# Optimization experiments

Hardware: AMD Instinct MI355X
Metric: run time of the kernel (lower is better)

The kernel has to match this reference:

```python
import jax, jax.numpy as jnp
import numpy as np

B, S, D, H = 4, 1024, 1024, 16
HD = D // H  # head_dim = 64
MASKED_BIAS = -10000.0


def setup_inputs() -> dict:
    key = jax.random.key(0)
    ks = jax.random.split(key, 7)
    sc = 0.02
    return {
        "hidden_states": jax.random.normal(ks[0], (B, S, D), jnp.float32),
        "textual_key": jax.random.normal(ks[1], (B, H, S, HD), jnp.float32),
        "textual_value": jax.random.normal(ks[2], (B, H, S, HD), jnp.float32),
        "Wc": jax.random.normal(ks[3], (D, 3 * D), jnp.float32) * sc,  # Conv1D c_attn
        "bc": jnp.zeros((3 * D,), jnp.float32),
        "Wp": jax.random.normal(ks[4], (D, D), jnp.float32) * sc,  # Conv1D c_proj
        "bp": jnp.zeros((D,), jnp.float32),
    }


def reference(hidden_states, textual_key, textual_value, Wc, bc, Wp, bp):
    b, s, d = hidden_states.shape
    # Conv1D: x @ W + b, then split into q, k, v
    qkv = hidden_states @ Wc + bc  # [B,S,3D]
    q, k, v = jnp.split(qkv, 3, axis=-1)

    def split_heads(t):  # [B,S,D] -> [B,H,S,HD]
        return t.reshape(b, s, H, HD).transpose(0, 2, 1, 3)

    q, k, v = split_heads(q), split_heads(k), split_heads(v)

    # cross-key scores against textual past + fused elementwise self-term
    text_w = jnp.einsum("bhqd,bhkd->bhqk", q, textual_key)  # [B,H,S,S_kv]
    self_w = jnp.sum(q * k, axis=-1, keepdims=True)  # [B,H,S,1]
    attn_w = jnp.concatenate([text_w, self_w], axis=-1) / (HD ** 0.5)

    # nonResidual causal mask: bias[kl-ql:kl, 1:kl+1] (strict lower-tri since
    # columns are shifted by 1) concatenated with an always-true self column
    i = jnp.arange(s)
    causal = i[None, :] < i[:, None]  # [S,S_kv]: allow k < q (strict)
    mask = jnp.concatenate([causal, jnp.ones((s, 1), bool)], axis=-1)[None, None]
    attn_w = jnp.where(mask, attn_w, jnp.asarray(MASKED_BIAS, attn_w.dtype))
    attn_w = jax.nn.softmax(attn_w, axis=-1)

    w_rest, w_self = attn_w[..., :-1], attn_w[..., -1:]
    out = jnp.einsum("bhqk,bhkd->bhqd", w_rest, textual_value) + w_self * v

    out = out.transpose(0, 2, 1, 3).reshape(b, s, d)  # merge heads
    return out @ Wp + bp
```

## Files before the change

kernel.cpp:

```cpp
#include <hip/hip_runtime.h>

typedef __bf16 bf16_t;
typedef __bf16 bf16x8 __attribute__((ext_vector_type(8)));
typedef __bf16 bf16x4 __attribute__((ext_vector_type(4)));
typedef float f32x4 __attribute__((ext_vector_type(4)));

__device__ __forceinline__ void gl_lds16(const bf16_t* g, bf16_t* l) {
  __builtin_amdgcn_global_load_lds(
      (const __attribute__((address_space(1))) unsigned int*)g,
      (__attribute__((address_space(3))) unsigned int*)l, 16, 0, 0);
}

__global__ __launch_bounds__(256) void prep_kernel(
    const float* __restrict__ hs, const float* __restrict__ tk, const float* __restrict__ tv,
    const float* __restrict__ Wc, const float* __restrict__ Wp,
    bf16_t* __restrict__ Ahs, bf16_t* __restrict__ Ktb, bf16_t* __restrict__ Vtb,
    bf16_t* __restrict__ WcT, bf16_t* __restrict__ WpT) {
  const int blk = blockIdx.x;
  if (blk < 8192) {
    const float4* src = (blk < 4096) ? (const float4*)hs : (const float4*)tk;
    bf16x4* dst = (blk < 4096) ? (bf16x4*)Ahs : (bf16x4*)Ktb;
    int i = (blk & 4095) * 256 + threadIdx.x;
    float4 v = src[i];
    bf16x4 o;
    o[0] = (bf16_t)v.x; o[1] = (bf16_t)v.y; o[2] = (bf16_t)v.z; o[3] = (bf16_t)v.w;
    dst[i] = o;
  } else {
    __shared__ float tile[32][33];
    const int x = threadIdx.x & 31, y0 = threadIdx.x >> 5;
    const float* in; bf16_t* out; int R, C, c0, r0; size_t base;
    if (blk < 11264) {
      int t = blk - 8192; in = Wc; out = WcT; R = 1024; C = 3072; base = 0;
      c0 = (t % 96) * 32; r0 = (t / 96) * 32;
    } else if (blk < 12288) {
      int t = blk - 11264; in = Wp; out = WpT; R = 1024; C = 1024; base = 0;
      c0 = (t & 31) * 32; r0 = (t >> 5) * 32;
    } else {
      int t = blk - 12288; int z = t >> 6, rest = t & 63;
      in = tv; out = Vtb; R = 1024; C = 64; base = (size_t)z * 65536;
      c0 = (rest & 1) * 32; r0 = (rest >> 1) * 32;
    }
#pragma unroll
    for (int k = 0; k < 4; k++) {
      int y = y0 + 8 * k;
      tile[y][x] = in[base + (size_t)(r0 + y) * C + c0 + x];
    }
    __syncthreads();
#pragma unroll
    for (int k = 0; k < 4; k++) {
      int y = y0 + 8 * k;
      out[base + (size_t)(c0 + y) * R + r0 + x] = (bf16_t)tile[x][y];
    }
  }
}

__global__ __launch_bounds__(256) void gemm_qkv_kernel(
    const bf16_t* __restrict__ A, const bf16_t* __restrict__ Bt, const float* __restrict__ bias,
    bf16_t* __restrict__ Qo, bf16_t* __restrict__ Ko, bf16_t* __restrict__ Vo) {
  __shared__ __align__(16) bf16_t Asm[128 * 64];
  __shared__ __align__(16) bf16_t Bsm[128 * 64];
  const int tid = threadIdx.x;
  const int wave = tid >> 6, lane = tid & 63;
  const int c = lane & 15, qd = lane >> 4;
  const int wm = (wave & 1) * 64, wn = (wave >> 1) * 64;
  const int id = blockIdx.y * 24 + blockIdx.x;
  const int xcd = id & 7, idx = id >> 3;
  const int n0 = (xcd * 3 + (idx % 3)) * 128, m0 = (idx / 3) * 128;

  f32x4 acc[4][4];
#pragma unroll
  for (int i = 0; i < 4; i++)
#pragma unroll
    for (int j = 0; j < 4; j++) acc[i][j] = (f32x4){0.f, 0.f, 0.f, 0.f};

  for (int kt = 0; kt < 1024; kt += 64) {
#pragma unroll
    for (int p = 0; p < 4; p++) {
      int chunk = p * 256 + tid;
      int row = chunk >> 3, sb = chunk & 7;
      int kb = sb ^ (row & 7);
      gl_lds16(A + (size_t)(m0 + row) * 1024 + kt + kb * 8, &Asm[chunk * 8]);
      gl_lds16(Bt + (size_t)(n0 + row) * 1024 + kt + kb * 8, &Bsm[chunk * 8]);
    }
    __syncthreads();
#pragma unroll
    for (int kk = 0; kk < 2; kk++) {
      bf16x8 af[4], bfr[4];
#pragma unroll
      for (int i = 0; i < 4; i++) {
        int row = wm + 16 * i + c;
        af[i] = *(const bf16x8*)(&Asm[row * 64 + (((4 * kk + qd) ^ (row & 7)) << 3)]);
      }
#pragma unroll
      for (int j = 0; j < 4; j++) {
        int row = wn + 16 * j + c;
        bfr[j] = *(const bf16x8*)(&Bsm[row * 64 + (((4 * kk + qd) ^ (row & 7)) << 3)]);
      }
#pragma unroll
      for (int i = 0; i < 4; i++)
#pragma unroll
        for (int j = 0; j < 4; j++)
          acc[i][j] = __builtin_amdgcn_mfma_f32_16x16x32_bf16(af[i], bfr[j], acc[i][j], 0, 0, 0);
    }
    __syncthreads();
  }
#pragma unroll
  for (int j = 0; j < 4; j++) {
    int n = n0 + wn + 16 * j + c;
    float bv = bias[n];
    int type = n >> 10, d = n & 1023;
    int h = d >> 6, hd = d & 63;
    bf16_t* dst = (type == 0) ? Qo : (type == 1) ? Ko : Vo;
#pragma unroll
    for (int i = 0; i < 4; i++) {
#pragma unroll
      for (int r = 0; r < 4; r++) {
        int m = m0 + wm + 16 * i + 4 * qd + r;
        int bb = m >> 10, s = m & 1023;
        dst[(((size_t)bb * 16 + h) * 1024 + s) * 64 + hd] = (bf16_t)(acc[i][j][r] + bv);
      }
    }
  }
}

__global__ __launch_bounds__(256) void gemm_out_kernel(
    const bf16_t* __restrict__ A, const bf16_t* __restrict__ Bt, const float* __restrict__ bias,
    float* __restrict__ out) {
  __shared__ bf16_t Asm[2][8192];
  __shared__ bf16_t Bsm[2][8192];
  const int tid = threadIdx.x;
  const int wave = tid >> 6, lane = tid & 63;
  const int c = lane & 15, qd = lane >> 4;
  const int wm = (wave & 1) * 64, wn = (wave >> 1) * 64;
  const int m0 = blockIdx.y * 128, n0 = blockIdx.x * 128;

  f32x4 acc[4][4];
#pragma unroll
  for (int i = 0; i < 4; i++)
#pragma unroll
    for (int j = 0; j < 4; j++) acc[i][j] = (f32x4){0.f, 0.f, 0.f, 0.f};

#pragma unroll
  for (int p = 0; p < 4; p++) {
    int chunk = p * 256 + tid;
    int row = chunk >> 3, sb = chunk & 7;
    int kb = sb ^ (row & 7);
    gl_lds16(A + (size_t)(m0 + row) * 1024 + kb * 8, &Asm[0][chunk * 8]);
    gl_lds16(Bt + (size_t)(n0 + row) * 1024 + kb * 8, &Bsm[0][chunk * 8]);
  }
  for (int it = 0; it < 16; it++) {
    __syncthreads();
    if (it < 15) {
      int nbuf = (it + 1) & 1, kt = (it + 1) * 64;
#pragma unroll
      for (int p = 0; p < 4; p++) {
        int chunk = p * 256 + tid;
        int row = chunk >> 3, sb = chunk & 7;
        int kb = sb ^ (row & 7);
        gl_lds16(A + (size_t)(m0 + row) * 1024 + kt + kb * 8, &Asm[nbuf][chunk * 8]);
        gl_lds16(Bt + (size_t)(n0 + row) * 1024 + kt + kb * 8, &Bsm[nbuf][chunk * 8]);
      }
    }
    const int bs = it & 1;
#pragma unroll
    for (int kk = 0; kk < 2; kk++) {
      bf16x8 af[4], bfr[4];
#pragma unroll
      for (int i = 0; i < 4; i++) {
        int row = wm + 16 * i + c;
        af[i] = *(const bf16x8*)(&Asm[bs][row * 64 + (((4 * kk + qd) ^ (row & 7)) << 3)]);
      }
#pragma unroll
      for (int j = 0; j < 4; j++) {
        int row = wn + 16 * j + c;
        bfr[j] = *(const bf16x8*)(&Bsm[bs][row * 64 + (((4 * kk + qd) ^ (row & 7)) << 3)]);
      }
#pragma unroll
      for (int i = 0; i < 4; i++)
#pragma unroll
        for (int j = 0; j < 4; j++)
          acc[i][j] = __builtin_amdgcn_mfma_f32_16x16x32_bf16(af[i], bfr[j], acc[i][j], 0, 0, 0);
    }
  }
#pragma unroll
  for (int j = 0; j < 4; j++) {
    int n = n0 + wn + 16 * j + c;
    float bv = bias[n];
#pragma unroll
    for (int i = 0; i < 4; i++) {
#pragma unroll
      for (int r = 0; r < 4; r++) {
        int m = m0 + wm + 16 * i + 4 * qd + r;
        out[(size_t)m * 1024 + n] = acc[i][j][r] + bv;
      }
    }
  }
}

#define ATTN_M 12.0f
__global__ __launch_bounds__(512) void attn_kernel(
    const bf16_t* __restrict__ Q, const bf16_t* __restrict__ K, const bf16_t* __restrict__ V,
    const bf16_t* __restrict__ Ktxt, const bf16_t* __restrict__ VtxtT,
    bf16_t* __restrict__ Aout) {
  const int bh = blockIdx.x;
  const int qt = blockIdx.y;
  const int b = bh >> 4, h = bh & 15;
  const int tid = threadIdx.x, wave = tid >> 6, lane = tid & 63;
  const int c = lane & 15, qd = lane >> 4;
  const int i_base = qt * 128 + wave * 16;
  const int kt_max = 2 * qt + 1;

  const bf16_t* Qb = Q + (size_t)bh * 65536;
  const bf16_t* Kb = K + (size_t)bh * 65536;
  const bf16_t* Vb = V + (size_t)bh * 65536;
  const bf16_t* Ktb = Ktxt + (size_t)bh * 65536;
  const bf16_t* Vtb = VtxtT + (size_t)bh * 65536;

  __shared__ bf16_t Ksm[2][4096];
  __shared__ bf16_t Vsm[2][4096];
  __shared__ bf16_t Psm[8][1024];

  {
    int row = tid >> 3, sb = tid & 7, kb = sb ^ (row & 7);
    gl_lds16(Ktb + (size_t)row * 64 + kb * 8, &Ksm[0][tid * 8]);
    gl_lds16(Vtb + (size_t)row * 1024 + kb * 8, &Vsm[0][tid * 8]);
  }

  bf16x8 aq[2], kf0, kf1;
  {
    const size_t ro = (size_t)(i_base + c) * 64;
    aq[0] = *(const bf16x8*)(Qb + ro + 8 * qd);
    aq[1] = *(const bf16x8*)(Qb + ro + 32 + 8 * qd);
    kf0 = *(const bf16x8*)(Kb + ro + 8 * qd);
    kf1 = *(const bf16x8*)(Kb + ro + 32 + 8 * qd);
  }
  float part = 0.f;
#pragma unroll
  for (int jj = 0; jj < 8; jj++)
    part += (float)aq[0][jj] * (float)kf0[jj] + (float)aq[1][jj] * (float)kf1[jj];
  part += __shfl_xor(part, 16, 64);
  part += __shfl_xor(part, 32, 64);

  float wself[4], l_part[4];
  f32x4 O[4];
#pragma unroll
  for (int r = 0; r < 4; r++) {
    wself[r] = __expf(__shfl(part, 4 * qd + r, 64) * 0.125f - ATTN_M);
    l_part[r] = 0.f;
  }
#pragma unroll
  for (int t = 0; t < 4; t++)
#pragma unroll
    for (int r = 0; r < 4; r++)
      O[t][r] = wself[r] * (float)Vb[(size_t)(i_base + 4 * qd + r) * 64 + 16 * t + c];

  for (int kt = 0; kt <= kt_max; kt++) {
    __syncthreads();
    if (kt < kt_max) {
      int nb = (kt + 1) & 1;
      int row = tid >> 3, sb = tid & 7, kb = sb ^ (row & 7);
      gl_lds16(Ktb + (size_t)((kt + 1) * 64 + row) * 64 + kb * 8, &Ksm[nb][tid * 8]);
      gl_lds16(Vtb + (size_t)row * 1024 + (kt + 1) * 64 + kb * 8, &Vsm[nb][tid * 8]);
    }
    if (64 * kt >= i_base + 16) continue;
    const int bs = kt & 1;

    f32x4 sc[4];
#pragma unroll
    for (int t = 0; t < 4; t++) sc[t] = (f32x4){0.f, 0.f, 0.f, 0.f};
#pragma unroll
    for (int kk = 0; kk < 2; kk++) {
#pragma unroll
      for (int t = 0; t < 4; t++) {
        int row = 16 * t + c;
        bf16x8 bk = *(const bf16x8*)(&Ksm[bs][row * 64 + (((4 * kk + qd) ^ (row & 7)) << 3)]);
        sc[t] = __builtin_amdgcn_mfma_f32_16x16x32_bf16(aq[kk], bk, sc[t], 0, 0, 0);
      }
    }
    const bool edge = (64 * kt + 63 >= i_base);
    if (!edge) {
#pragma unroll
      for (int t = 0; t < 4; t++)
#pragma unroll
        for (int r = 0; r < 4; r++) {
          float p = __expf(sc[t][r] * 0.125f - ATTN_M);
          l_part[r] += p;
          sc[t][r] = p;
        }
    } else {
#pragma unroll
      for (int t = 0; t < 4; t++)
#pragma unroll
        for (int r = 0; r < 4; r++) {
          bool masked = (64 * kt + 16 * t + c >= i_base + 4 * qd + r);
          float p = masked ? 0.f : __expf(sc[t][r] * 0.125f - ATTN_M);
          l_part[r] += p;
          sc[t][r] = p;
        }
    }
#pragma unroll
    for (int t = 0; t < 4; t++) {
#pragma unroll
      for (int r = 0; r < 4; r++) {
        int row = 4 * qd + r;
        int col = 16 * t + c;
        Psm[wave][row * 64 + (((col >> 3) ^ (row & 7)) << 3) + (col & 7)] = (bf16_t)sc[t][r];
      }
    }
#pragma unroll
    for (int kk = 0; kk < 2; kk++) {
      bf16x8 ap = *(const bf16x8*)(&Psm[wave][c * 64 + (((4 * kk + qd) ^ (c & 7)) << 3)]);
#pragma unroll
      for (int u = 0; u < 4; u++) {
        int row = 16 * u + c;
        bf16x8 bv = *(const bf16x8*)(&Vsm[bs][row * 64 + (((4 * kk + qd) ^ (row & 7)) << 3)]);
        O[u] = __builtin_amdgcn_mfma_f32_16x16x32_bf16(ap, bv, O[u], 0, 0, 0);
      }
    }
  }

#pragma unroll
  for (int r = 0; r < 4; r++) {
#pragma unroll
    for (int mk = 1; mk < 16; mk <<= 1) l_part[r] += __shfl_xor(l_part[r], mk, 64);
    float inv = 1.0f / (l_part[r] + wself[r]);
    int i = i_base + 4 * qd + r;
#pragma unroll
    for (int u = 0; u < 4; u++)
      Aout[((size_t)b * 1024 + i) * 1024 + h * 64 + 16 * u + c] = (bf16_t)(O[u][r] * inv);
  }
}

extern "C" void kernel_launch(void* const* d_in, const int* in_sizes, int n_in,
                              void* d_out, int out_size, void* d_ws, size_t ws_size,
                              hipStream_t stream) {
  const float* hs = (const float*)d_in[0];
  const float* tk = (const float*)d_in[1];
  const float* tv = (const float*)d_in[2];
  const float* Wc = (const float*)d_in[3];
  const float* bc = (const float*)d_in[4];
  const float* Wp = (const float*)d_in[5];
  const float* bp = (const float*)d_in[6];
  float* out = (float*)d_out;

  bf16_t* ws = (bf16_t*)d_ws;
  const size_t M1 = 1u << 20;
  bf16_t* Ahs  = ws;
  bf16_t* WcT  = ws + 4 * M1;
  bf16_t* WpT  = ws + 7 * M1;
  bf16_t* Ktb  = ws + 8 * M1;
  bf16_t* Vtb  = ws + 12 * M1;
  bf16_t* Qb   = ws + 16 * M1;
  bf16_t* Kb   = ws + 20 * M1;
  bf16_t* Vb   = ws + 24 * M1;
  bf16_t* Aout = ws + 28 * M1;

  prep_kernel<<<16384, 256, 0, stream>>>(hs, tk, tv, Wc, Wp, Ahs, Ktb, Vtb, WcT, WpT);
  gemm_qkv_kernel<<<dim3(24, 32), 256, 0, stream>>>(Ahs, WcT, bc, Qb, Kb, Vb);
  attn_kernel<<<dim3(64, 8), 512, 0, stream>>>(Qb, Kb, Vb, Ktb, Vtb, Aout);
  gemm_out_kernel<<<dim3(8, 32), 256, 0, stream>>>(Aout, WpT, bp, out);
}
```

Baseline: 203.4 us.

## Keep attention probabilities in registers via transposed scores; shrink out-proj tile

The attention kernel now computes the transposed score tile (K as the A operand), so each lane's probabilities already match the A-operand layout of an fp16 16x16x16 MFMA. This removes the per-wave LDS round trip for P. Textual V is converted to fp16 during prep to match that instruction. Separately, the output projection GEMM uses 64x128 tiles with twice as many blocks, to improve occupancy and CU coverage for a GEMM with few blocks.

```diff
diff --git a/kernel.cpp b/kernel.cpp
--- a/kernel.cpp
+++ b/kernel.cpp
@@ -3,9 +3,10 @@
 typedef __bf16 bf16_t;
 typedef __bf16 bf16x8 __attribute__((ext_vector_type(8)));
 typedef __bf16 bf16x4 __attribute__((ext_vector_type(4)));
+typedef _Float16 f16x4 __attribute__((ext_vector_type(4)));
 typedef float f32x4 __attribute__((ext_vector_type(4)));
 
-__device__ __forceinline__ void gl_lds16(const bf16_t* g, bf16_t* l) {
+__device__ __forceinline__ void gl_lds16(const void* g, void* l) {
   __builtin_amdgcn_global_load_lds(
       (const __attribute__((address_space(1))) unsigned int*)g,
       (__attribute__((address_space(3))) unsigned int*)l, 16, 0, 0);
@@ -14,7 +15,7 @@
 __global__ __launch_bounds__(256) void prep_kernel(
     const float* __restrict__ hs, const float* __restrict__ tk, const float* __restrict__ tv,
     const float* __restrict__ Wc, const float* __restrict__ Wp,
-    bf16_t* __restrict__ Ahs, bf16_t* __restrict__ Ktb, bf16_t* __restrict__ Vtb,
+    bf16_t* __restrict__ Ahs, bf16_t* __restrict__ Ktb, _Float16* __restrict__ Vtb,
     bf16_t* __restrict__ WcT, bf16_t* __restrict__ WpT) {
   const int blk = blockIdx.x;
   if (blk < 8192) {
@@ -28,16 +29,16 @@
   } else {
     __shared__ float tile[32][33];
     const int x = threadIdx.x & 31, y0 = threadIdx.x >> 5;
-    const float* in; bf16_t* out; int R, C, c0, r0; size_t base;
+    const float* in; bf16_t* out; int C, c0, r0; size_t base; bool isV = false;
     if (blk < 11264) {
-      int t = blk - 8192; in = Wc; out = WcT; R = 1024; C = 3072; base = 0;
+      int t = blk - 8192; in = Wc; out = WcT; C = 3072; base = 0;
       c0 = (t % 96) * 32; r0 = (t / 96) * 32;
     } else if (blk < 12288) {
-      int t = blk - 11264; in = Wp; out = WpT; R = 1024; C = 1024; base = 0;
+      int t = blk - 11264; in = Wp; out = WpT; C = 1024; base = 0;
       c0 = (t & 31) * 32; r0 = (t >> 5) * 32;
     } else {
       int t = blk - 12288; int z = t >> 6, rest = t & 63;
-      in = tv; out = Vtb; R = 1024; C = 64; base = (size_t)z * 65536;
+      in = tv; out = nullptr; isV = true; C = 64; base = (size_t)z * 65536;
       c0 = (rest & 1) * 32; r0 = (rest >> 1) * 32;
     }
 #pragma unroll
@@ -49,7 +50,10 @@
 #pragma unroll
     for (int k = 0; k < 4; k++) {
       int y = y0 + 8 * k;
-      out[base + (size_t)(c0 + y) * R + r0 + x] = (bf16_t)tile[x][y];
+      if (isV)
+        Vtb[base + (size_t)(c0 + y) * 1024 + r0 + x] = (_Float16)tile[x][y];
+      else
+        out[base + (size_t)(c0 + y) * 1024 + r0 + x] = (bf16_t)tile[x][y];
     }
   }
 }
@@ -126,26 +130,30 @@
 __global__ __launch_bounds__(256) void gemm_out_kernel(
     const bf16_t* __restrict__ A, const bf16_t* __restrict__ Bt, const float* __restrict__ bias,
     float* __restrict__ out) {
-  __shared__ bf16_t Asm[2][8192];
+  __shared__ bf16_t Asm[2][4096];
   __shared__ bf16_t Bsm[2][8192];
   const int tid = threadIdx.x;
   const int wave = tid >> 6, lane = tid & 63;
   const int c = lane & 15, qd = lane >> 4;
-  const int wm = (wave & 1) * 64, wn = (wave >> 1) * 64;
-  const int m0 = blockIdx.y * 128, n0 = blockIdx.x * 128;
-
-  f32x4 acc[4][4];
+  const int wn = wave * 32;
+  const int m0 = blockIdx.y * 64, n0 = blockIdx.x * 128;
+
+  f32x4 acc[4][2];
 #pragma unroll
   for (int i = 0; i < 4; i++)
 #pragma unroll
-    for (int j = 0; j < 4; j++) acc[i][j] = (f32x4){0.f, 0.f, 0.f, 0.f};
-
+    for (int j = 0; j < 2; j++) acc[i][j] = (f32x4){0.f, 0.f, 0.f, 0.f};
+
+#pragma unroll
+  for (int p = 0; p < 2; p++) {
+    int chunk = p * 256 + tid;
+    int row = chunk >> 3, sb = chunk & 7, kb = sb ^ (row & 7);
+    gl_lds16(A + (size_t)(m0 + row) * 1024 + kb * 8, &Asm[0][chunk * 8]);
+  }
 #pragma unroll
   for (int p = 0; p < 4; p++) {
     int chunk = p * 256 + tid;
-    int row = chunk >> 3, sb = chunk & 7;
-    int kb = sb ^ (row & 7);
-    gl_lds16(A + (size_t)(m0 + row) * 1024 + kb * 8, &Asm[0][chunk * 8]);
+    int row = chunk >> 3, sb = chunk & 7, kb = sb ^ (row & 7);
     gl_lds16(Bt + (size_t)(n0 + row) * 1024 + kb * 8, &Bsm[0][chunk * 8]);
   }
   for (int it = 0; it < 16; it++) {
@@ -153,44 +161,48 @@
     if (it < 15) {
       int nbuf = (it + 1) & 1, kt = (it + 1) * 64;
 #pragma unroll
+      for (int p = 0; p < 2; p++) {
+        int chunk = p * 256 + tid;
+        int row = chunk >> 3, sb = chunk & 7, kb = sb ^ (row & 7);
+        gl_lds16(A + (size_t)(m0 + row) * 1024 + kt + kb * 8, &Asm[nbuf][chunk * 8]);
+      }
+#pragma unroll
       for (int p = 0; p < 4; p++) {
         int chunk = p * 256 + tid;
-        int row = chunk >> 3, sb = chunk & 7;
-        int kb = sb ^ (row & 7);
-        gl_lds16(A + (size_t)(m0 + row) * 1024 + kt + kb * 8, &Asm[nbuf][chunk * 8]);
+        int row = chunk >> 3, sb = chunk & 7, kb = sb ^ (row & 7);
         gl_lds16(Bt + (size_t)(n0 + row) * 1024 + kt + kb * 8, &Bsm[nbuf][chunk * 8]);
       }
     }
     const int bs = it & 1;
 #pragma unroll
     for (int kk = 0; kk < 2; kk++) {
-      bf16x8 af[4], bfr[4];
+      bf16x8 af[4], bfr[2];
 #pragma unroll
       for (int i = 0; i < 4; i++) {
-        int row = wm + 16 * i + c;
+        int row = 16 * i + c;
         af[i] = *(const bf16x8*)(&Asm[bs][row * 64 + (((4 * kk + qd) ^ (row & 7)) << 3)]);
       }
 #pragma unroll
-      for (int j = 0; j < 4; j++) {
+      for (int j = 0; j < 2; j++) {
         int row = wn + 16 * j + c;
         bfr[j] = *(const bf16x8*)(&Bsm[bs][row * 64 + (((4 * kk + qd) ^ (row & 7)) << 3)]);
       }
 #pragma unroll
       for (int i = 0; i < 4; i++)
 #pragma unroll
-        for (int j = 0; j < 4; j++)
+        for (int j = 0; j < 2; j++)
           acc[i][j] = __builtin_amdgcn_mfma_f32_16x16x32_bf16(af[i], bfr[j], acc[i][j], 0, 0, 0);
     }
   }
 #pragma unroll
-  for (int j = 0; j < 4; j++) {
+  for (int j = 0; j < 2; j++) {
     int n = n0 + wn + 16 * j + c;
     float bv = bias[n];
 #pragma unroll
     for (int i = 0; i < 4; i++) {
 #pragma unroll
       for (int r = 0; r < 4; r++) {
-        int m = m0 + wm + 16 * i + 4 * qd + r;
+        int m = m0 + 16 * i + 4 * qd + r;
         out[(size_t)m * 1024 + n] = acc[i][j][r] + bv;
       }
     }
@@ -200,7 +212,7 @@
 #define ATTN_M 12.0f
 __global__ __launch_bounds__(512) void attn_kernel(
     const bf16_t* __restrict__ Q, const bf16_t* __restrict__ K, const bf16_t* __restrict__ V,
-    const bf16_t* __restrict__ Ktxt, const bf16_t* __restrict__ VtxtT,
+    const bf16_t* __restrict__ Ktxt, const _Float16* __restrict__ VtxtT,
     bf16_t* __restrict__ Aout) {
   const int bh = blockIdx.x;
   const int qt = blockIdx.y;
@@ -214,11 +226,10 @@
   const bf16_t* Kb = K + (size_t)bh * 65536;
   const bf16_t* Vb = V + (size_t)bh * 65536;
   const bf16_t* Ktb = Ktxt + (size_t)bh * 65536;
-  const bf16_t* Vtb = VtxtT + (size_t)bh * 65536;
+  const _Float16* Vtb = VtxtT + (size_t)bh * 65536;
 
   __shared__ bf16_t Ksm[2][4096];
-  __shared__ bf16_t Vsm[2][4096];
-  __shared__ bf16_t Psm[8][1024];
+  __shared__ _Float16 Vsm[2][4096];
 
   {
     int row = tid >> 3, sb = tid & 7, kb = sb ^ (row & 7);
@@ -241,18 +252,17 @@
   part += __shfl_xor(part, 16, 64);
   part += __shfl_xor(part, 32, 64);
 
-  float wself[4], l_part[4];
+  float wself[4];
+  float l_loc = 0.f;
   f32x4 O[4];
 #pragma unroll
-  for (int r = 0; r < 4; r++) {
+  for (int r = 0; r < 4; r++)
     wself[r] = __expf(__shfl(part, 4 * qd + r, 64) * 0.125f - ATTN_M);
-    l_part[r] = 0.f;
-  }
-#pragma unroll
-  for (int t = 0; t < 4; t++)
+#pragma unroll
+  for (int u = 0; u < 4; u++)
 #pragma unroll
     for (int r = 0; r < 4; r++)
-      O[t][r] = wself[r] * (float)Vb[(size_t)(i_base + 4 * qd + r) * 64 + 16 * t + c];
+      O[u][r] = wself[r] * (float)Vb[(size_t)(i_base + 4 * qd + r) * 64 + 16 * u + c];
 
   for (int kt = 0; kt <= kt_max; kt++) {
     __syncthreads();
@@ -274,56 +284,49 @@
       for (int t = 0; t < 4; t++) {
         int row = 16 * t + c;
         bf16x8 bk = *(const bf16x8*)(&Ksm[bs][row * 64 + (((4 * kk + qd) ^ (row & 7)) << 3)]);
-        sc[t] = __builtin_amdgcn_mfma_f32_16x16x32_bf16(aq[kk], bk, sc[t], 0, 0, 0);
+        sc[t] = __builtin_amdgcn_mfma_f32_16x16x32_bf16(bk, aq[kk], sc[t], 0, 0, 0);
       }
     }
     const bool edge = (64 * kt + 63 >= i_base);
+    f16x4 pa[4];
     if (!edge) {
 #pragma unroll
       for (int t = 0; t < 4; t++)
 #pragma unroll
         for (int r = 0; r < 4; r++) {
           float p = __expf(sc[t][r] * 0.125f - ATTN_M);
-          l_part[r] += p;
-          sc[t][r] = p;
+          l_loc += p;
+          pa[t][r] = (_Float16)p;
         }
     } else {
 #pragma unroll
       for (int t = 0; t < 4; t++)
 #pragma unroll
         for (int r = 0; r < 4; r++) {
-          bool masked = (64 * kt + 16 * t + c >= i_base + 4 * qd + r);
+          bool masked = (64 * kt + 16 * t + 4 * qd + r >= i_base + c);
           float p = masked ? 0.f : __expf(sc[t][r] * 0.125f - ATTN_M);
-          l_part[r] += p;
-          sc[t][r] = p;
+          l_loc += p;
+          pa[t][r] = (_Float16)p;
         }
     }
 #pragma unroll
-    for (int t = 0; t < 4; t++) {
-#pragma unroll
-      for (int r = 0; r < 4; r++) {
-        int row = 4 * qd + r;
-        int col = 16 * t + c;
-        Psm[wave][row * 64 + (((col >> 3) ^ (row & 7)) << 3) + (col & 7)] = (bf16_t)sc[t][r];
-      }
-    }
-#pragma unroll
-    for (int kk = 0; kk < 2; kk++) {
-      bf16x8 ap = *(const bf16x8*)(&Psm[wave][c * 64 + (((4 * kk + qd) ^ (c & 7)) << 3)]);
-#pragma unroll
-      for (int u = 0; u < 4; u++) {
-        int row = 16 * u + c;
-        bf16x8 bv = *(const bf16x8*)(&Vsm[bs][row * 64 + (((4 * kk + qd) ^ (row & 7)) << 3)]);
-        O[u] = __builtin_amdgcn_mfma_f32_16x16x32_bf16(ap, bv, O[u], 0, 0, 0);
-      }
-    }
-  }
-
+    for (int u = 0; u < 4; u++) {
+      int row = 16 * u + c;
+#pragma unroll
+      for (int t = 0; t < 4; t++) {
+        int kc = 2 * t + (qd >> 1);
+        f16x4 vb = *(const f16x4*)(&Vsm[bs][row * 64 + ((kc ^ (row & 7)) << 3) + ((qd & 1) << 2)]);
+        O[u] = __builtin_amdgcn_mfma_f32_16x16x16f16(pa[t], vb, O[u], 0, 0, 0);
+      }
+    }
+  }
+
+  l_loc += __shfl_xor(l_loc, 16, 64);
+  l_loc += __shfl_xor(l_loc, 32, 64);
 #pragma unroll
   for (int r = 0; r < 4; r++) {
-#pragma unroll
-    for (int mk = 1; mk < 16; mk <<= 1) l_part[r] += __shfl_xor(l_part[r], mk, 64);
-    float inv = 1.0f / (l_part[r] + wself[r]);
+    float lq = __shfl(l_loc, 4 * qd + r, 16);
+    float inv = 1.0f / (lq + wself[r]);
     int i = i_base + 4 * qd + r;
 #pragma unroll
     for (int u = 0; u < 4; u++)
@@ -349,7 +352,7 @@
   bf16_t* WcT  = ws + 4 * M1;
   bf16_t* WpT  = ws + 7 * M1;
   bf16_t* Ktb  = ws + 8 * M1;
-  bf16_t* Vtb  = ws + 12 * M1;
+  _Float16* Vtb = (_Float16*)(ws + 12 * M1);
   bf16_t* Qb   = ws + 16 * M1;
   bf16_t* Kb   = ws + 20 * M1;
   bf16_t* Vb   = ws + 24 * M1;
@@ -358,5 +361,5 @@
   prep_kernel<<<16384, 256, 0, stream>>>(hs, tk, tv, Wc, Wp, Ahs, Ktb, Vtb, WcT, WpT);
   gemm_qkv_kernel<<<dim3(24, 32), 256, 0, stream>>>(Ahs, WcT, bc, Qb, Kb, Vb);
   attn_kernel<<<dim3(64, 8), 512, 0, stream>>>(Qb, Kb, Vb, Ktb, Vtb, Aout);
-  gemm_out_kernel<<<dim3(8, 32), 256, 0, stream>>>(Aout, WpT, bp, out);
-}
+  gemm_out_kernel<<<dim3(8, 64), 256, 0, stream>>>(Aout, WpT, bp, out);
+}
```

After: 200.1 us. No clear change (-1.6%).
